# Performance work log

Hardware: AMD Instinct MI355X
Metric: run time of the kernel (lower is better)

Reference implementation:

```python
import jax, jax.numpy as jnp
import numpy as np


def setup_inputs() -> dict:
    key = jax.random.key(0)
    k1, k2 = jax.random.split(key)
    NUM_INS, NUM_CLASS = 8192, 5000
    # probabilities strictly inside (0,1) so log terms are finite
    output = jax.random.uniform(k1, (NUM_INS, NUM_CLASS), dtype=jnp.float32,
                                minval=1e-6, maxval=1.0 - 1e-6)
    # labels in {0,1,2}; 2 == ignore
    target = jax.random.randint(k2, (NUM_INS, NUM_CLASS), 0, 3, dtype=jnp.int64)
    return {"output": output, "target": target}


def reference(output, target):
    is_pos = target == 1
    is_neg = target == 0
    # masked BCE: -log(p) for positives, -log(1-p) for negatives, 0 where target==2
    per_elem = jnp.where(is_pos, -jnp.log(output),
                         jnp.where(is_neg, -jnp.log1p(-output), 0.0))
    count = jnp.sum(is_pos | is_neg)
    cost = jnp.sum(per_elem) / count.astype(per_elem.dtype)
    return cost
```

## Files before the change

kernel.cpp:

```cpp
#include <hip/hip_runtime.h>


#define GRID_BLOCKS 2048
#define BLOCK 256

__global__ __launch_bounds__(BLOCK) void bce_reduce_kernel(
    const float* __restrict__ prob,
    const int* __restrict__ tgt,
    float* __restrict__ part_sum,
    unsigned int* __restrict__ part_cnt,
    int n)
{
    const int tid    = blockIdx.x * BLOCK + threadIdx.x;
    const int stride = GRID_BLOCKS * BLOCK;

    const int n4  = n >> 2;
    const int n4h = n4 >> 1;

    float        lsum = 0.0f;
    unsigned int lcnt = 0u;

    const float4* __restrict__ p4 = (const float4*)prob;
    const int4*   __restrict__ t4 = (const int4*)tgt;

    for (int i = tid; i < n4h; i += stride) {
        float4 pa = p4[i];
        int4   ta = t4[i];
        float4 pb = p4[i + n4h];
        int4   tb = t4[i + n4h];

        #define ACC(P, T)                                   \
        {                                                   \
            float v = ((T) == 1) ? (P) : 1.0f - (P);        \
            bool  c = (unsigned)(T) <= 1u;                  \
            float l = -__logf(v);                           \
            lsum += c ? l : 0.0f;                           \
            lcnt += c ? 1u : 0u;                            \
        }
        ACC(pa.x, ta.x) ACC(pa.y, ta.y) ACC(pa.z, ta.z) ACC(pa.w, ta.w)
        ACC(pb.x, tb.x) ACC(pb.y, tb.y) ACC(pb.z, tb.z) ACC(pb.w, tb.w)
    }

    for (int i = (n4h * 2) * 4 + tid; i < n; i += stride) {
        float p = prob[i];
        int   t = tgt[i];
        float v = (t == 1) ? p : 1.0f - p;
        bool  c = (unsigned)t <= 1u;
        float l = -__logf(v);
        lsum += c ? l : 0.0f;
        lcnt += c ? 1u : 0u;
    }

    #pragma unroll
    for (int off = 32; off > 0; off >>= 1) {
        lsum += __shfl_down(lsum, off, 64);
        lcnt += __shfl_down(lcnt, off, 64);
    }

    __shared__ float        s_sum[4];
    __shared__ unsigned int s_cnt[4];
    const int lane = threadIdx.x & 63;
    const int wave = threadIdx.x >> 6;
    if (lane == 0) { s_sum[wave] = lsum; s_cnt[wave] = lcnt; }
    __syncthreads();
    if (threadIdx.x == 0) {
        part_sum[blockIdx.x] = s_sum[0] + s_sum[1] + s_sum[2] + s_sum[3];
        part_cnt[blockIdx.x] = s_cnt[0] + s_cnt[1] + s_cnt[2] + s_cnt[3];
    }
}

__global__ __launch_bounds__(BLOCK) void bce_finalize_kernel(
    const float* __restrict__ part_sum,
    const unsigned int* __restrict__ part_cnt,
    float* __restrict__ out)
{
    float        lsum = 0.0f;
    unsigned int lcnt = 0u;
    for (int i = threadIdx.x; i < GRID_BLOCKS; i += BLOCK) {
        lsum += part_sum[i];
        lcnt += part_cnt[i];
    }
    #pragma unroll
    for (int off = 32; off > 0; off >>= 1) {
        lsum += __shfl_down(lsum, off, 64);
        lcnt += __shfl_down(lcnt, off, 64);
    }
    __shared__ float        s_sum[4];
    __shared__ unsigned int s_cnt[4];
    const int lane = threadIdx.x & 63;
    const int wave = threadIdx.x >> 6;
    if (lane == 0) { s_sum[wave] = lsum; s_cnt[wave] = lcnt; }
    __syncthreads();
    if (threadIdx.x == 0) {
        float        bsum = s_sum[0] + s_sum[1] + s_sum[2] + s_sum[3];
        unsigned int bcnt = s_cnt[0] + s_cnt[1] + s_cnt[2] + s_cnt[3];
        out[0] = bsum / (float)bcnt;
    }
}

extern "C" void kernel_launch(void* const* d_in, const int* in_sizes, int n_in,
                              void* d_out, int out_size, void* d_ws, size_t ws_size,
                              hipStream_t stream) {
    const float* prob = (const float*)d_in[0];
    const int*   tgt  = (const int*)d_in[1];
    float*       out  = (float*)d_out;

    const int n = in_sizes[0];

    float*        part_sum = (float*)d_ws;
    unsigned int* part_cnt = (unsigned int*)((char*)d_ws + GRID_BLOCKS * sizeof(float));

    bce_reduce_kernel<<<GRID_BLOCKS, BLOCK, 0, stream>>>(prob, tgt, part_sum, part_cnt, n);
    bce_finalize_kernel<<<1, BLOCK, 0, stream>>>(part_sum, part_cnt, out);
}
```

Before: 329.7 us.

## Deepen per-thread memory parallelism with 8-way unrolled strided loads, fewer blocks

Replaces the two-halves load pattern with an 8-way unrolled grid-stride loop that issues eight float4/int4 load pairs before computing, and cuts the grid from 2048 to 1000 blocks. The aim is more outstanding memory requests per thread to keep HBM saturated on a bandwidth-bound reduction, plus a smaller partial-reduction array. Costs are higher register use and fewer waves, which could lower occupancy, and remainder loops for elements that do not fill a full unrolled step.

```diff
diff --git a/kernel.cpp b/kernel.cpp
--- a/kernel.cpp
+++ b/kernel.cpp
@@ -1,8 +1,9 @@
 #include <hip/hip_runtime.h>
 
 
-#define GRID_BLOCKS 2048
+#define GRID_BLOCKS 1000
 #define BLOCK 256
+#define UNROLL 8
 
 __global__ __launch_bounds__(BLOCK) void bce_reduce_kernel(
     const float* __restrict__ prob,
@@ -13,9 +14,7 @@
 {
     const int tid    = blockIdx.x * BLOCK + threadIdx.x;
     const int stride = GRID_BLOCKS * BLOCK;
-
-    const int n4  = n >> 2;
-    const int n4h = n4 >> 1;
+    const int n4     = n >> 2;
 
     float        lsum = 0.0f;
     unsigned int lcnt = 0u;
@@ -23,32 +22,39 @@
     const float4* __restrict__ p4 = (const float4*)prob;
     const int4*   __restrict__ t4 = (const int4*)tgt;
 
-    for (int i = tid; i < n4h; i += stride) {
-        float4 pa = p4[i];
-        int4   ta = t4[i];
-        float4 pb = p4[i + n4h];
-        int4   tb = t4[i + n4h];
+    #define ACC(P, T)                                   \
+    {                                                   \
+        float v = ((T) == 1) ? (P) : 1.0f - (P);        \
+        bool  c = (unsigned)(T) <= 1u;                  \
+        float l = -__logf(v);                           \
+        lsum += c ? l : 0.0f;                           \
+        lcnt += c ? 1u : 0u;                            \
+    }
+    #define ACC4(P, T) ACC((P).x,(T).x) ACC((P).y,(T).y) ACC((P).z,(T).z) ACC((P).w,(T).w)
 
-        #define ACC(P, T)                                   \
-        {                                                   \
-            float v = ((T) == 1) ? (P) : 1.0f - (P);        \
-            bool  c = (unsigned)(T) <= 1u;                  \
-            float l = -__logf(v);                           \
-            lsum += c ? l : 0.0f;                           \
-            lcnt += c ? 1u : 0u;                            \
+    int i = tid;
+    for (; i + (UNROLL - 1) * stride < n4; i += UNROLL * stride) {
+        float4 p[UNROLL];
+        int4   t[UNROLL];
+        #pragma unroll
+        for (int j = 0; j < UNROLL; ++j) {
+            p[j] = p4[i + j * stride];
+            t[j] = t4[i + j * stride];
         }
-        ACC(pa.x, ta.x) ACC(pa.y, ta.y) ACC(pa.z, ta.z) ACC(pa.w, ta.w)
-        ACC(pb.x, tb.x) ACC(pb.y, tb.y) ACC(pb.z, tb.z) ACC(pb.w, tb.w)
+        #pragma unroll
+        for (int j = 0; j < UNROLL; ++j) {
+            ACC4(p[j], t[j])
+        }
     }
-
-    for (int i = (n4h * 2) * 4 + tid; i < n; i += stride) {
-        float p = prob[i];
-        int   t = tgt[i];
-        float v = (t == 1) ? p : 1.0f - p;
-        bool  c = (unsigned)t <= 1u;
-        float l = -__logf(v);
-        lsum += c ? l : 0.0f;
-        lcnt += c ? 1u : 0u;
+    for (; i < n4; i += stride) {
+        float4 p = p4[i];
+        int4   t = t4[i];
+        ACC4(p, t)
+    }
+    for (int k = (n4 << 2) + tid; k < n; k += stride) {
+        float p = prob[k];
+        int   t = tgt[k];
+        ACC(p, t)
     }
 
     #pragma unroll
```

New measurement: 330.5 us. About the same (+0.2%).
